# Kernel optimization log

Measured on AMD Instinct MI355X. Metric: run time of the kernel, lower is better.

## Reference

```python
import jax, jax.numpy as jnp
import numpy as np

B, LK, D, H = 16, 4096, 1024, 16
DK = D // H
EPS = 1e-5
NEG = -1.0e9


def _layernorm(x, g, b):
    m = jnp.mean(x, axis=-1, keepdims=True)
    v = jnp.mean((x - m) ** 2, axis=-1, keepdims=True)
    return (x - m) * jax.lax.rsqrt(v + EPS) * g + b


def setup_inputs() -> dict:
    key0 = jax.random.key(0)
    ks = jax.random.split(key0, 12)

    def lin(k, fan_in, fan_out):
        # torch nn.Linear default-ish scale; stored as [in, out] so y = x @ W + b
        return jax.random.normal(k, (fan_in, fan_out), jnp.float32) / np.float32(np.sqrt(fan_in))

    return {
        "query": jax.random.normal(ks[0], (B, 1, D), jnp.float32),
        "key": jax.random.normal(ks[1], (B, LK, D), jnp.float32),
        "mask": jax.random.randint(ks[2], (B, 1, LK), 0, 2, jnp.int32),
        "Wq": lin(ks[3], D, D), "bq": jnp.zeros((D,), jnp.float32),
        "Wk": lin(ks[4], D, D), "bk": jnp.zeros((D,), jnp.float32),
        "Wv": lin(ks[5], D, D), "bv": jnp.zeros((D,), jnp.float32),
        "Wo": lin(ks[6], D, D), "bo": jnp.zeros((D,), jnp.float32),
        "raw_thr": jnp.full((H, 1, 1), 0.1, jnp.float32),
        "Wvp": lin(ks[7], 2 * D, D),  # v_proj, no bias
        "W1": lin(ks[8], D, 2 * D), "b1": jnp.zeros((2 * D,), jnp.float32),
        "W2": lin(ks[9], 2 * D, D), "b2": jnp.zeros((D,), jnp.float32),
        "g1": jnp.ones((D,), jnp.float32), "be1": jnp.zeros((D,), jnp.float32),
        "g2": jnp.ones((D,), jnp.float32), "be2": jnp.zeros((D,), jnp.float32),
    }


def reference(query, key, mask, Wq, bq, Wk, bk, Wv, bv, Wo, bo, raw_thr,
              Wvp, W1, b1, W2, b2, g1, be1, g2, be2):
    b = query.shape[0]
    lk = key.shape[1]
    # v = cat(key, query.repeat(1, Lk, 1)) @ Wvp   (query has seq_len 1)
    v_in = jnp.concatenate([key, jnp.broadcast_to(query, (b, lk, D))], axis=2)
    v = v_in @ Wvp  # [B, Lk, D]

    Q = (query @ Wq + bq).reshape(b, 1, H, DK).transpose(0, 2, 1, 3)   # [B,H,1,DK]
    K = (key @ Wk + bk).reshape(b, lk, H, DK).transpose(0, 2, 1, 3)    # [B,H,Lk,DK]
    V = (v @ Wv + bv).reshape(b, lk, H, DK).transpose(0, 2, 1, 3)      # [B,H,Lk,DK]

    scores = jnp.einsum("bhqd,bhkd->bhqk", Q, K) / jnp.sqrt(jnp.float32(DK))
    # padding mask: [B,1,Lk] -> [B,1,1,Lk]
    scores = jnp.where(mask[:, None] == 0, NEG, scores)
    # learned per-head threshold: softplus(raw_thr) -> [1,H,1,1]
    thr = jax.nn.softplus(raw_thr)[None]
    scores = jnp.where(scores <= thr, NEG, scores)
    attn = jax.nn.softmax(scores, axis=-1)

    x = jnp.einsum("bhqk,bhkd->bhqd", attn, V)            # [B,H,1,DK]
    x = x.transpose(0, 2, 1, 3).reshape(b, 1, H * DK)      # [B,1,D]
    attn_out = x @ Wo + bo

    x = _layernorm(query + attn_out, g1, be1)
    ff = jax.nn.relu(x @ W1 + b1) @ W2 + b2
    x = _layernorm(x + ff, g2, be2)
    return x
```

## Files before the change

kernel.cpp:

```cpp
#include <hip/hip_runtime.h>
#include <hip/hip_bf16.h>

#define NB 16
#define NHD 16
#define ND 1024
#define NLK 4096
#define NFF 2048

typedef float f32x4 __attribute__((ext_vector_type(4)));
typedef __bf16 bf16x4v __attribute__((ext_vector_type(4)));
typedef __bf16 bf16x8 __attribute__((ext_vector_type(8)));

__global__ void k_fill(float* out, int n, float v) {
  int i = blockIdx.x * 256 + threadIdx.x;
  if (i < n) out[i] = v;
}

__global__ __launch_bounds__(256) void k0t(const float* __restrict__ Wvp,
                                           __hip_bfloat16* __restrict__ wvpt) {
  int n0 = blockIdx.x * 64, k0 = blockIdx.y * 64;
  int t = threadIdx.x;
  __shared__ float ts[64][68];
#pragma unroll
  for (int i = 0; i < 4; ++i) {
    int idx = t * 4 + i * 1024;
    int kk = idx >> 6, nn = idx & 63;
    float4 v = *(const float4*)(Wvp + (size_t)(k0 + kk) * ND + n0 + nn);
    ts[kk][nn] = v.x; ts[kk][nn + 1] = v.y; ts[kk][nn + 2] = v.z; ts[kk][nn + 3] = v.w;
  }
  __syncthreads();
#pragma unroll
  for (int i = 0; i < 4; ++i) {
    int idx = t * 4 + i * 1024;
    int nn = idx >> 6, kk = idx & 63;
    bf16x4v o;
#pragma unroll
    for (int j = 0; j < 4; ++j) o[j] = (__bf16)ts[kk + j][nn];
    *(bf16x4v*)((__bf16*)wvpt + (size_t)(n0 + nn) * ND + k0 + kk) = o;
  }
}

__global__ __launch_bounds__(256) void k0a(const float* __restrict__ Wq,
                                           const float* __restrict__ bq,
                                           const float* __restrict__ Wvp,
                                           const float* __restrict__ query,
                                           float* __restrict__ Qrow,
                                           float* __restrict__ cvec) {
  int which = blockIdx.z;
  int j = blockIdx.x * 256 + threadIdx.x;
  int i0 = blockIdx.y * 64;
  int t = threadIdx.x;
  __shared__ float qs[64][20];
  {
    int e = t * 4;
    int b = e >> 6, ii = e & 63;
    float4 v = *(const float4*)(query + (size_t)b * ND + i0 + ii);
    qs[ii][b] = v.x; qs[ii + 1][b] = v.y; qs[ii + 2][b] = v.z; qs[ii + 3][b] = v.w;
  }
  __syncthreads();
  float acc[16];
#pragma unroll
  for (int q = 0; q < 16; ++q) acc[q] = 0.f;
  for (int ii = 0; ii < 64; ++ii) {
    int i = i0 + ii;
    float wv = which ? Wvp[(size_t)(ND + i) * ND + j] : Wq[(size_t)i * ND + j];
    float qv[16];
    const float4* qp = (const float4*)&qs[ii][0];
    *(float4*)&qv[0] = qp[0];
    *(float4*)&qv[4] = qp[1];
    *(float4*)&qv[8] = qp[2];
    *(float4*)&qv[12] = qp[3];
#pragma unroll
    for (int q = 0; q < 16; ++q) acc[q] += wv * qv[q];
  }
  float* out = which ? cvec : Qrow;
  float bias = (!which && blockIdx.y == 0) ? bq[j] : 0.f;
#pragma unroll
  for (int q = 0; q < 16; ++q) atomicAdd(&out[q * ND + j], acc[q] + bias);
}

__global__ __launch_bounds__(256) void k0b(const float* __restrict__ Wk,
                                           const float* __restrict__ bk,
                                           const float* __restrict__ Qrow,
                                           __hip_bfloat16* __restrict__ t_bf,
                                           float* __restrict__ s0) {
  int h = blockIdx.x;
  int d0 = blockIdx.y * 128;
  int t = threadIdx.x;
  __shared__ float qs[16 * 64];
  __shared__ float wks[128 * 66];
  {
    int lin = t * 4;
    int b = lin >> 6, dk = lin & 63;
    *(float4*)&qs[b * 64 + dk] = *(const float4*)(Qrow + b * ND + h * 64 + dk);
  }
#pragma unroll
  for (int e = 0; e < 8; ++e) {
    int lin = e * 1024 + t * 4;
    int d = lin >> 6, dk = lin & 63;
    *(float4*)&wks[d * 66 + dk] = *(const float4*)(Wk + (size_t)(d0 + d) * ND + h * 64 + dk);
  }
  __syncthreads();
  if (blockIdx.y == 0 && t < 16) {
    float a = 0.f;
    const float* bkh = bk + h * 64;
    for (int jj = 0; jj < 64; ++jj) a += bkh[jj] * qs[t * 64 + jj];
    s0[t * 16 + h] = a;
  }
  int d = t >> 1, bh = (t & 1) * 8;
  float acc[8];
#pragma unroll
  for (int q = 0; q < 8; ++q) acc[q] = 0.f;
  for (int dk = 0; dk < 64; ++dk) {
    float wv = wks[d * 66 + dk];
#pragma unroll
    for (int q = 0; q < 8; ++q) acc[q] += wv * qs[(bh + q) * 64 + dk];
  }
#pragma unroll
  for (int q = 0; q < 8; ++q)
    t_bf[(size_t)((bh + q) * 16 + h) * ND + d0 + d] = (__hip_bfloat16)acc[q];
}

__global__ __launch_bounds__(256) void k_flash(const float* __restrict__ key,
                                               const __hip_bfloat16* __restrict__ t_bf,
                                               const float* __restrict__ s0,
                                               const float* __restrict__ raw_thr,
                                               const int* __restrict__ mask,
                                               float* __restrict__ pu,
                                               float* __restrict__ mloc,
                                               float* __restrict__ lloc) {
  int ch = blockIdx.x, b = blockIdx.y;
  int t = threadIdx.x;
  int wv = t >> 6, lane = t & 63, l15 = lane & 15, g4 = lane >> 4;
  __shared__ float ps[4][32][17];
  __shared__ float wls[32][16];
  __shared__ float red[16][16];
  __shared__ float mrun[16], lrun[16], fact[16], mnew_s[16], thv_s[16], s0_s[16];
  f32x4 pu_r[16];
#pragma unroll
  for (int h = 0; h < 16; ++h) pu_r[h] = (f32x4){0.f, 0.f, 0.f, 0.f};
  if (t < 16) {
    mrun[t] = -1.0e9f;
    lrun[t] = 0.f;
    thv_s[t] = log1pf(expf(raw_thr[t]));
    s0_s[t] = s0[b * 16 + t];
  }
  __syncthreads();
  const float* keyb = key + (size_t)b * NLK * ND;
  const __hip_bfloat16* tb = t_bf + (size_t)(b * 16 + l15) * ND;
  int dsl = wv * 256;
  int dlane = dsl + lane * 4;
  int k0c = ch * 128;
  for (int sp = 0; sp < 4; ++sp) {
    int ks0 = k0c + sp * 32;
    f32x4 acc0 = {0.f, 0.f, 0.f, 0.f}, acc1 = {0.f, 0.f, 0.f, 0.f};
    for (int st = 0; st < 8; ++st) {
      int d = dsl + st * 32 + g4 * 8;
      bf16x8 bfr = *(const bf16x8*)(tb + d);
      const float* a0p = keyb + (size_t)(ks0 + l15) * ND + d;
      const float* a1p = a0p + (size_t)16 * ND;
      float a0[8], a1[8];
      *(float4*)&a0[0] = *(const float4*)a0p;
      *(float4*)&a0[4] = *(const float4*)(a0p + 4);
      *(float4*)&a1[0] = *(const float4*)a1p;
      *(float4*)&a1[4] = *(const float4*)(a1p + 4);
      bf16x8 af0, af1;
#pragma unroll
      for (int j = 0; j < 8; ++j) {
        af0[j] = (__bf16)a0[j];
        af1[j] = (__bf16)a1[j];
      }
      acc0 = __builtin_amdgcn_mfma_f32_16x16x32_bf16(af0, bfr, acc0, 0, 0, 0);
      acc1 = __builtin_amdgcn_mfma_f32_16x16x32_bf16(af1, bfr, acc1, 0, 0, 0);
    }
#pragma unroll
    for (int r = 0; r < 4; ++r) {
      ps[wv][g4 * 4 + r][l15] = acc0[r];
      ps[wv][16 + g4 * 4 + r][l15] = acc1[r];
    }
    __syncthreads();
    int kk0 = t >> 4, hh = t & 15;
    float sv0, sv1;
    {
      float s = (ps[0][kk0][hh] + ps[1][kk0][hh] + ps[2][kk0][hh] + ps[3][kk0][hh] +
                 s0_s[hh]) * 0.125f;
      int mv = mask[b * NLK + ks0 + kk0];
      sv0 = (mv != 0 && s > thv_s[hh]) ? s : -1.0e9f;
    }
    {
      int k2 = kk0 + 16;
      float s = (ps[0][k2][hh] + ps[1][k2][hh] + ps[2][k2][hh] + ps[3][k2][hh] +
                 s0_s[hh]) * 0.125f;
      int mv = mask[b * NLK + ks0 + k2];
      sv1 = (mv != 0 && s > thv_s[hh]) ? s : -1.0e9f;
    }
    red[kk0][hh] = fmaxf(sv0, sv1);
    __syncthreads();
    for (int s2 = 8; s2 > 0; s2 >>= 1) {
      if (kk0 < s2) red[kk0][hh] = fmaxf(red[kk0][hh], red[kk0 + s2][hh]);
      __syncthreads();
    }
    if (t < 16) {
      float mn = fmaxf(mrun[t], red[0][t]);
      mnew_s[t] = mn;
      fact[t] = expf(mrun[t] - mn);
      mrun[t] = mn;
    }
    __syncthreads();
    float w0 = expf(sv0 - mnew_s[hh]);
    float w1 = expf(sv1 - mnew_s[hh]);
    wls[kk0][hh] = w0;
    wls[kk0 + 16][hh] = w1;
    red[kk0][hh] = w0 + w1;
    __syncthreads();
    for (int s2 = 8; s2 > 0; s2 >>= 1) {
      if (kk0 < s2) red[kk0][hh] += red[kk0 + s2][hh];
      __syncthreads();
    }
    if (t < 16) lrun[t] = lrun[t] * fact[t] + red[0][t];
#pragma unroll
    for (int h = 0; h < 16; ++h) pu_r[h] *= fact[h];
    const float* kb2 = keyb + (size_t)ks0 * ND + dlane;
    for (int k = 0; k < 32; ++k) {
      f32x4 kv = *(const f32x4*)(kb2 + (size_t)k * ND);
#pragma unroll
      for (int h = 0; h < 16; ++h) pu_r[h] += wls[k][h] * kv;
    }
    __syncthreads();
  }
  size_t pubase = (size_t)((b * 32 + ch) * 16) * ND + dlane;
#pragma unroll
  for (int h = 0; h < 16; ++h) *(f32x4*)(pu + pubase + (size_t)h * ND) = pu_r[h];
  if (t < 16) {
    mloc[(b * 32 + ch) * 16 + t] = mrun[t];
    lloc[(b * 32 + ch) * 16 + t] = lrun[t];
  }
}

__global__ __launch_bounds__(256) void k_ured(const float* __restrict__ pu,
                                              const float* __restrict__ mloc,
                                              const float* __restrict__ lloc,
                                              __hip_bfloat16* __restrict__ u_bf) {
  int h = blockIdx.x, b = blockIdx.y;
  int t = threadIdx.x;
  __shared__ float sc_s[32];
  if (t < 32) {
    float m = mloc[(b * 32 + t) * 16 + h];
    float l = lloc[(b * 32 + t) * 16 + h];
    float mg = m;
    for (int o = 16; o > 0; o >>= 1) mg = fmaxf(mg, __shfl_xor(mg, o, 32));
    float term = l * expf(m - mg);
    float ls = term;
    for (int o = 16; o > 0; o >>= 1) ls += __shfl_xor(ls, o, 32);
    sc_s[t] = expf(m - mg) / ls;
  }
  __syncthreads();
  int d = t * 4;
  f32x4 acc = {0.f, 0.f, 0.f, 0.f};
  for (int c = 0; c < 32; ++c) {
    f32x4 v = *(const f32x4*)(pu + (size_t)((b * 32 + c) * 16 + h) * ND + d);
    acc += sc_s[c] * v;
  }
  bf16x4v o;
#pragma unroll
  for (int j = 0; j < 4; ++j) o[j] = (__bf16)acc[j];
  *(bf16x4v*)((__bf16*)u_bf + (size_t)(b * 16 + h) * ND + d) = o;
}

__global__ __launch_bounds__(256) void k_zm(const __hip_bfloat16* __restrict__ u_bf,
                                            const __hip_bfloat16* __restrict__ wvpt,
                                            float* __restrict__ z) {
  int ntg = blockIdx.x, mt = blockIdx.y;
  int t = threadIdx.x, wv = t >> 6, lane = t & 63, l15 = lane & 15, g4 = lane >> 4;
  int nt = ntg * 4 + wv;
  const __hip_bfloat16* ub = u_bf + (size_t)(mt * 16 + l15) * ND;
  const __hip_bfloat16* wb = wvpt + (size_t)(nt * 16 + l15) * ND;
  f32x4 acc = {0.f, 0.f, 0.f, 0.f};
  for (int ks = 0; ks < 32; ++ks) {
    int d = ks * 32 + g4 * 8;
    bf16x8 a = *(const bf16x8*)(ub + d);
    bf16x8 bb = *(const bf16x8*)(wb + d);
    acc = __builtin_amdgcn_mfma_f32_16x16x32_bf16(a, bb, acc, 0, 0, 0);
  }
#pragma unroll
  for (int r = 0; r < 4; ++r)
    z[(size_t)(mt * 16 + g4 * 4 + r) * ND + nt * 16 + l15] = acc[r];
}

__global__ __launch_bounds__(256) void k_attnx(const float* __restrict__ z,
                                               const float* __restrict__ cvec,
                                               const float* __restrict__ Wv,
                                               const float* __restrict__ bv,
                                               float* __restrict__ attn_x) {
  __shared__ float vb[16 * 132];
  int h = blockIdx.x;
  int d0 = blockIdx.y * 128;
  int t = threadIdx.x;
#pragma unroll
  for (int e = 0; e < 8; ++e) {
    int lin = e * 256 + t;
    int bb = lin >> 7, dd = lin & 127;
    vb[bb * 132 + dd] =
        z[(size_t)(bb * 16 + h) * ND + d0 + dd] + cvec[(size_t)bb * ND + d0 + dd];
  }
  __syncthreads();
  int joff = t & 63, bg = t >> 6;
  int j = h * 64 + joff;
  float acc[4] = {0.f, 0.f, 0.f, 0.f};
  for (int dd = 0; dd < 128; ++dd) {
    float wv = Wv[(size_t)(d0 + dd) * ND + j];
#pragma unroll
    for (int q = 0; q < 4; ++q) acc[q] += wv * vb[(bg * 4 + q) * 132 + dd];
  }
#pragma unroll
  for (int q = 0; q < 4; ++q) {
    float val = acc[q];
    if (blockIdx.y == 0) val += bv[j];
    atomicAdd(&attn_x[(size_t)(bg * 4 + q) * ND + j], val);
  }
}

__global__ __launch_bounds__(256) void k_r1(const float* __restrict__ attn_x,
                                            const float* __restrict__ Wo,
                                            const float* __restrict__ bo,
                                            const float* __restrict__ query,
                                            float* __restrict__ r1) {
  __shared__ float ax[16 * 68];
  int j0 = blockIdx.x * 128;
  int d0 = blockIdx.y * 64;
  int t = threadIdx.x;
  {
    int lin = t * 4;
    int bb = lin >> 6, dd = lin & 63;
    *(float4*)&ax[bb * 68 + dd] = *(const float4*)(attn_x + (size_t)bb * ND + d0 + dd);
  }
  __syncthreads();
  int joff = t & 127, bg = t >> 7;
  int j = j0 + joff;
  float acc[8];
#pragma unroll
  for (int q = 0; q < 8; ++q) acc[q] = 0.f;
  for (int dd = 0; dd < 64; ++dd) {
    float wv = Wo[(size_t)(d0 + dd) * ND + j];
#pragma unroll
    for (int q = 0; q < 8; ++q) acc[q] += wv * ax[(bg * 8 + q) * 68 + dd];
  }
#pragma unroll
  for (int q = 0; q < 8; ++q) {
    int bb = bg * 8 + q;
    float val = acc[q];
    if (blockIdx.y == 0) val += bo[j] + query[(size_t)bb * ND + j];
    atomicAdd(&r1[(size_t)bb * ND + j], val);
  }
}

__global__ __launch_bounds__(256) void k_ff1(const float* __restrict__ r1,
                                             const float* __restrict__ g1,
                                             const float* __restrict__ be1,
                                             const float* __restrict__ W1,
                                             float* __restrict__ h1) {
  int n = blockIdx.x * 256 + threadIdx.x;
  int d0 = blockIdx.y * 64;
  int t = threadIdx.x;
  __shared__ float mv_s[16], iv_s[16];
  __shared__ float xs[16 * 68];
  {
    int row = t >> 4, seg = t & 15;
    float s = 0.f, s2 = 0.f;
    const float* rp = r1 + (size_t)row * ND + seg * 64;
    for (int q = 0; q < 16; ++q) {
      float4 v = *(const float4*)(rp + q * 4);
      s += v.x + v.y + v.z + v.w;
      s2 += v.x * v.x + v.y * v.y + v.z * v.z + v.w * v.w;
    }
    for (int o = 1; o < 16; o <<= 1) {
      s += __shfl_xor(s, o, 16);
      s2 += __shfl_xor(s2, o, 16);
    }
    if (seg == 0) {
      float mean = s * (1.f / ND);
      float var = s2 * (1.f / ND) - mean * mean;
      mv_s[row] = mean;
      iv_s[row] = rsqrtf(var + 1e-5f);
    }
  }
  __syncthreads();
  {
    int e = t * 4;
    int bb = e >> 6, dd = e & 63;
    float4 v = *(const float4*)(r1 + (size_t)bb * ND + d0 + dd);
    float4 g = *(const float4*)(g1 + d0 + dd);
    float4 be = *(const float4*)(be1 + d0 + dd);
    float m = mv_s[bb], iv = iv_s[bb];
    xs[bb * 68 + dd] = (v.x - m) * iv * g.x + be.x;
    xs[bb * 68 + dd + 1] = (v.y - m) * iv * g.y + be.y;
    xs[bb * 68 + dd + 2] = (v.z - m) * iv * g.z + be.z;
    xs[bb * 68 + dd + 3] = (v.w - m) * iv * g.w + be.w;
  }
  __syncthreads();
  float acc[16];
#pragma unroll
  for (int q = 0; q < 16; ++q) acc[q] = 0.f;
  for (int dd = 0; dd < 64; ++dd) {
    float wv = W1[(size_t)(d0 + dd) * NFF + n];
#pragma unroll
    for (int q = 0; q < 16; ++q) acc[q] += wv * xs[q * 68 + dd];
  }
#pragma unroll
  for (int q = 0; q < 16; ++q) atomicAdd(&h1[(size_t)q * NFF + n], acc[q]);
}

__global__ __launch_bounds__(256) void k_ff2(const float* __restrict__ h1,
                                             const float* __restrict__ b1,
                                             const float* __restrict__ W2,
                                             float* __restrict__ out2) {
  __shared__ float hs[16 * 132];
  int j0 = blockIdx.x * 128;
  int n0 = blockIdx.y * 128;
  int t = threadIdx.x;
#pragma unroll
  for (int e = 0; e < 8; ++e) {
    int lin = e * 256 + t;
    int bb = lin >> 7, nn = lin & 127;
    float hv = h1[(size_t)bb * NFF + n0 + nn] + b1[n0 + nn];
    hs[bb * 132 + nn] = fmaxf(hv, 0.f);
  }
  __syncthreads();
  int joff = t & 127, bg = t >> 7;
  int j = j0 + joff;
  float acc[8];
#pragma unroll
  for (int q = 0; q < 8; ++q) acc[q] = 0.f;
  for (int nn = 0; nn < 128; ++nn) {
    float wv = W2[(size_t)(n0 + nn) * ND + j];
#pragma unroll
    for (int q = 0; q < 8; ++q) acc[q] += wv * hs[(bg * 8 + q) * 132 + nn];
  }
#pragma unroll
  for (int q = 0; q < 8; ++q) atomicAdd(&out2[(size_t)(bg * 8 + q) * ND + j], acc[q]);
}

__global__ __launch_bounds__(256) void k_ln2(const float* __restrict__ r1,
                                             const float* __restrict__ g1,
                                             const float* __restrict__ be1,
                                             const float* __restrict__ out2,
                                             const float* __restrict__ b2,
                                             const float* __restrict__ g2,
                                             const float* __restrict__ be2,
                                             float* __restrict__ outp) {
  int b = blockIdx.x, t = threadIdx.x;
  __shared__ float rs[256], rs2[256];
  float4 v = *(const float4*)(r1 + (size_t)b * ND + t * 4);
  float s = v.x + v.y + v.z + v.w;
  float s2 = v.x * v.x + v.y * v.y + v.z * v.z + v.w * v.w;
  rs[t] = s;
  rs2[t] = s2;
  __syncthreads();
  for (int st = 128; st > 0; st >>= 1) {
    if (t < st) {
      rs[t] += rs[t + st];
      rs2[t] += rs2[t + st];
    }
    __syncthreads();
  }
  float mean = rs[0] * (1.f / ND);
  float var = rs2[0] * (1.f / ND) - mean * mean;
  float inv = rsqrtf(var + 1e-5f);
  float4 g = *(const float4*)(g1 + t * 4);
  float4 be = *(const float4*)(be1 + t * 4);
  float4 o2 = *(const float4*)(out2 + (size_t)b * ND + t * 4);
  float4 bb2 = *(const float4*)(b2 + t * 4);
  float4 v2;
  v2.x = (v.x - mean) * inv * g.x + be.x + o2.x + bb2.x;
  v2.y = (v.y - mean) * inv * g.y + be.y + o2.y + bb2.y;
  v2.z = (v.z - mean) * inv * g.z + be.z + o2.z + bb2.z;
  v2.w = (v.w - mean) * inv * g.w + be.w + o2.w + bb2.w;
  __syncthreads();
  s = v2.x + v2.y + v2.z + v2.w;
  s2 = v2.x * v2.x + v2.y * v2.y + v2.z * v2.z + v2.w * v2.w;
  rs[t] = s;
  rs2[t] = s2;
  __syncthreads();
  for (int st = 128; st > 0; st >>= 1) {
    if (t < st) {
      rs[t] += rs[t + st];
      rs2[t] += rs2[t + st];
    }
    __syncthreads();
  }
  float mean2 = rs[0] * (1.f / ND);
  float var2 = rs2[0] * (1.f / ND) - mean2 * mean2;
  float inv2 = rsqrtf(var2 + 1e-5f);
  float4 gg = *(const float4*)(g2 + t * 4);
  float4 bbe = *(const float4*)(be2 + t * 4);
  float4 o;
  o.x = (v2.x - mean2) * inv2 * gg.x + bbe.x;
  o.y = (v2.y - mean2) * inv2 * gg.y + bbe.y;
  o.z = (v2.z - mean2) * inv2 * gg.z + bbe.z;
  o.w = (v2.w - mean2) * inv2 * gg.w + bbe.w;
  *(float4*)(outp + (size_t)b * ND + t * 4) = o;
}

extern "C" void kernel_launch(void* const* d_in, const int* in_sizes, int n_in,
                              void* d_out, int out_size, void* d_ws, size_t ws_size,
                              hipStream_t stream) {
  const float* query = (const float*)d_in[0];
  const float* key = (const float*)d_in[1];
  const int* mask = (const int*)d_in[2];
  const float* Wq = (const float*)d_in[3];
  const float* bq = (const float*)d_in[4];
  const float* Wk = (const float*)d_in[5];
  const float* bk = (const float*)d_in[6];
  const float* Wv = (const float*)d_in[7];
  const float* bv = (const float*)d_in[8];
  const float* Wo = (const float*)d_in[9];
  const float* bo = (const float*)d_in[10];
  const float* raw_thr = (const float*)d_in[11];
  const float* Wvp = (const float*)d_in[12];
  const float* W1 = (const float*)d_in[13];
  const float* b1 = (const float*)d_in[14];
  const float* W2 = (const float*)d_in[15];
  const float* b2 = (const float*)d_in[16];
  const float* g1 = (const float*)d_in[17];
  const float* be1 = (const float*)d_in[18];
  const float* g2 = (const float*)d_in[19];
  const float* be2 = (const float*)d_in[20];

  const size_t OFF_QROW = 0;
  const size_t OFF_C = 65536;
  const size_t OFF_ATTNX = 131072;
  const size_t OFF_R1 = 196608;
  const size_t OFF_H1 = 262144;
  const size_t OFF_OUT2 = 393216;
  const size_t ZERO_BYTES = 458752;
  const size_t OFF_S0 = 458752;
  const size_t OFF_MLOC = 459776;
  const size_t OFF_LLOC = 492544;
  const size_t OFF_TBF = 525312;
  const size_t OFF_UBF = 1049600;
  const size_t OFF_WVPT = 1573888;
  const size_t OFF_Z = 3671040;
  const size_t OFF_PU = 4719616;
  const size_t TOTAL = 38274048;

  if (ws_size < TOTAL) {
    k_fill<<<dim3((out_size + 255) / 256), dim3(256), 0, stream>>>((float*)d_out, out_size,
                                                                   12345.0f);
    return;
  }

  char* wsb = (char*)d_ws;
  float* Qrow = (float*)(wsb + OFF_QROW);
  float* cvec = (float*)(wsb + OFF_C);
  float* attn_x = (float*)(wsb + OFF_ATTNX);
  float* r1 = (float*)(wsb + OFF_R1);
  float* h1 = (float*)(wsb + OFF_H1);
  float* out2 = (float*)(wsb + OFF_OUT2);
  float* s0 = (float*)(wsb + OFF_S0);
  float* mloc = (float*)(wsb + OFF_MLOC);
  float* lloc = (float*)(wsb + OFF_LLOC);
  __hip_bfloat16* t_bf = (__hip_bfloat16*)(wsb + OFF_TBF);
  __hip_bfloat16* u_bf = (__hip_bfloat16*)(wsb + OFF_UBF);
  __hip_bfloat16* wvpt = (__hip_bfloat16*)(wsb + OFF_WVPT);
  float* z = (float*)(wsb + OFF_Z);
  float* pu = (float*)(wsb + OFF_PU);

  hipMemsetAsync(d_ws, 0, ZERO_BYTES, stream);

  k0t<<<dim3(16, 16), dim3(256), 0, stream>>>(Wvp, wvpt);
  k0a<<<dim3(4, 16, 2), dim3(256), 0, stream>>>(Wq, bq, Wvp, query, Qrow, cvec);
  k0b<<<dim3(16, 8), dim3(256), 0, stream>>>(Wk, bk, Qrow, t_bf, s0);
  k_flash<<<dim3(32, 16), dim3(256), 0, stream>>>(key, t_bf, s0, raw_thr, mask, pu, mloc, lloc);
  k_ured<<<dim3(16, 16), dim3(256), 0, stream>>>(pu, mloc, lloc, u_bf);
  k_zm<<<dim3(16, 16), dim3(256), 0, stream>>>(u_bf, wvpt, z);
  k_attnx<<<dim3(16, 8), dim3(256), 0, stream>>>(z, cvec, Wv, bv, attn_x);
  k_r1<<<dim3(8, 16), dim3(256), 0, stream>>>(attn_x, Wo, bo, query, r1);
  k_ff1<<<dim3(8, 16), dim3(256), 0, stream>>>(r1, g1, be1, W1, h1);
  k_ff2<<<dim3(8, 16), dim3(256), 0, stream>>>(h1, b1, W2, out2);
  k_ln2<<<dim3(16), dim3(256), 0, stream>>>(r1, g1, be1, out2, b2, g2, be2, (float*)d_out);
}
```

Before: 205.2 us.

## Fuse tail stages into persistent kernel with grid barriers; widen flash blocks

Merges the Wvp transpose and the query projections into one prep kernel. Seven tail kernels (u reduction, z GEMM, attn_x, r1, ff1, ff2, ln2) become a single 256-block kernel that uses atomic-counter grid barriers in place of kernel launches. k_flash now uses 512 threads with 8 waves, each covering half the d-slice, and its per-step max/sum reductions use wave shuffles instead of log-step shared-memory loops. This removes launch gaps and trims register pressure in flash. The grid barriers can deadlock if the 256 blocks are not all resident at once, and the flash block now has a larger cross-wave partial-sum reduction.

```diff
diff --git a/kernel.cpp b/kernel.cpp
--- a/kernel.cpp
+++ b/kernel.cpp
@@ -8,6 +8,7 @@
 #define NFF 2048
 
 typedef float f32x4 __attribute__((ext_vector_type(4)));
+typedef float f32x2 __attribute__((ext_vector_type(2)));
 typedef __bf16 bf16x4v __attribute__((ext_vector_type(4)));
 typedef __bf16 bf16x8 __attribute__((ext_vector_type(8)));
 
@@ -16,67 +17,91 @@
   if (i < n) out[i] = v;
 }
 
-__global__ __launch_bounds__(256) void k0t(const float* __restrict__ Wvp,
-                                           __hip_bfloat16* __restrict__ wvpt) {
-  int n0 = blockIdx.x * 64, k0 = blockIdx.y * 64;
+__device__ __forceinline__ void gbar(unsigned* ctr, unsigned nblk) {
+  __syncthreads();
+  if (threadIdx.x == 0) {
+    __threadfence();
+    __hip_atomic_fetch_add(ctr, 1u, __ATOMIC_ACQ_REL, __HIP_MEMORY_SCOPE_AGENT);
+    while (__hip_atomic_load(ctr, __ATOMIC_ACQUIRE, __HIP_MEMORY_SCOPE_AGENT) < nblk) {
+    }
+    __threadfence();
+  }
+  __syncthreads();
+}
+
+__global__ __launch_bounds__(256) void k_prep(const float* __restrict__ Wq,
+                                              const float* __restrict__ bq,
+                                              const float* __restrict__ Wvp,
+                                              const float* __restrict__ query,
+                                              float* __restrict__ Qrow,
+                                              float* __restrict__ cvec,
+                                              __hip_bfloat16* __restrict__ wvpt) {
+  __shared__ float pmem[64 * 68];
+  int blk = blockIdx.x;
   int t = threadIdx.x;
-  __shared__ float ts[64][68];
-#pragma unroll
-  for (int i = 0; i < 4; ++i) {
-    int idx = t * 4 + i * 1024;
-    int kk = idx >> 6, nn = idx & 63;
-    float4 v = *(const float4*)(Wvp + (size_t)(k0 + kk) * ND + n0 + nn);
-    ts[kk][nn] = v.x; ts[kk][nn + 1] = v.y; ts[kk][nn + 2] = v.z; ts[kk][nn + 3] = v.w;
-  }
-  __syncthreads();
-#pragma unroll
-  for (int i = 0; i < 4; ++i) {
-    int idx = t * 4 + i * 1024;
-    int nn = idx >> 6, kk = idx & 63;
-    bf16x4v o;
-#pragma unroll
-    for (int j = 0; j < 4; ++j) o[j] = (__bf16)ts[kk + j][nn];
-    *(bf16x4v*)((__bf16*)wvpt + (size_t)(n0 + nn) * ND + k0 + kk) = o;
-  }
-}
-
-__global__ __launch_bounds__(256) void k0a(const float* __restrict__ Wq,
-                                           const float* __restrict__ bq,
-                                           const float* __restrict__ Wvp,
-                                           const float* __restrict__ query,
-                                           float* __restrict__ Qrow,
-                                           float* __restrict__ cvec) {
-  int which = blockIdx.z;
-  int j = blockIdx.x * 256 + threadIdx.x;
-  int i0 = blockIdx.y * 64;
-  int t = threadIdx.x;
-  __shared__ float qs[64][20];
-  {
-    int e = t * 4;
-    int b = e >> 6, ii = e & 63;
-    float4 v = *(const float4*)(query + (size_t)b * ND + i0 + ii);
-    qs[ii][b] = v.x; qs[ii + 1][b] = v.y; qs[ii + 2][b] = v.z; qs[ii + 3][b] = v.w;
-  }
-  __syncthreads();
-  float acc[16];
-#pragma unroll
-  for (int q = 0; q < 16; ++q) acc[q] = 0.f;
-  for (int ii = 0; ii < 64; ++ii) {
-    int i = i0 + ii;
-    float wv = which ? Wvp[(size_t)(ND + i) * ND + j] : Wq[(size_t)i * ND + j];
-    float qv[16];
-    const float4* qp = (const float4*)&qs[ii][0];
-    *(float4*)&qv[0] = qp[0];
-    *(float4*)&qv[4] = qp[1];
-    *(float4*)&qv[8] = qp[2];
-    *(float4*)&qv[12] = qp[3];
-#pragma unroll
-    for (int q = 0; q < 16; ++q) acc[q] += wv * qv[q];
-  }
-  float* out = which ? cvec : Qrow;
-  float bias = (!which && blockIdx.y == 0) ? bq[j] : 0.f;
-#pragma unroll
-  for (int q = 0; q < 16; ++q) atomicAdd(&out[q * ND + j], acc[q] + bias);
+  if (blk < 128) {
+    int which = blk >> 6;
+    int jb = blk & 3;
+    int i0 = ((blk >> 2) & 15) * 64;
+    int j = jb * 256 + t;
+    {
+      int e = t * 4;
+      int b = e >> 6, ii = e & 63;
+      float4 v = *(const float4*)(query + (size_t)b * ND + i0 + ii);
+      pmem[ii * 20 + b] = v.x;
+      pmem[(ii + 1) * 20 + b] = v.y;
+      pmem[(ii + 2) * 20 + b] = v.z;
+      pmem[(ii + 3) * 20 + b] = v.w;
+    }
+    __syncthreads();
+    float acc[16];
+#pragma unroll
+    for (int q = 0; q < 16; ++q) acc[q] = 0.f;
+    for (int ii = 0; ii < 64; ++ii) {
+      int i = i0 + ii;
+      float wv = which ? Wvp[(size_t)(ND + i) * ND + j] : Wq[(size_t)i * ND + j];
+      float qv[16];
+      const float4* qp = (const float4*)&pmem[ii * 20];
+      *(float4*)&qv[0] = qp[0];
+      *(float4*)&qv[4] = qp[1];
+      *(float4*)&qv[8] = qp[2];
+      *(float4*)&qv[12] = qp[3];
+#pragma unroll
+      for (int q = 0; q < 16; ++q) acc[q] += wv * qv[q];
+    }
+    float* out = which ? cvec : Qrow;
+    float bias = (!which && i0 == 0) ? bq[j] : 0.f;
+#pragma unroll
+    for (int q = 0; q < 16; ++q) atomicAdd(&out[q * ND + j], acc[q] + bias);
+  } else {
+    int tb = blk - 128;
+    int n0 = (tb & 15) * 64;
+    int k0base = (tb >> 4) * 256;
+    for (int it = 0; it < 4; ++it) {
+      int k0 = k0base + it * 64;
+#pragma unroll
+      for (int i = 0; i < 4; ++i) {
+        int idx = t * 4 + i * 1024;
+        int kk = idx >> 6, nn = idx & 63;
+        float4 v = *(const float4*)(Wvp + (size_t)(k0 + kk) * ND + n0 + nn);
+        pmem[kk * 68 + nn] = v.x;
+        pmem[kk * 68 + nn + 1] = v.y;
+        pmem[kk * 68 + nn + 2] = v.z;
+        pmem[kk * 68 + nn + 3] = v.w;
+      }
+      __syncthreads();
+#pragma unroll
+      for (int i = 0; i < 4; ++i) {
+        int idx = t * 4 + i * 1024;
+        int nn = idx >> 6, kk = idx & 63;
+        bf16x4v o;
+#pragma unroll
+        for (int j = 0; j < 4; ++j) o[j] = (__bf16)pmem[(kk + j) * 68 + nn];
+        *(bf16x4v*)((__bf16*)wvpt + (size_t)(n0 + nn) * ND + k0 + kk) = o;
+      }
+      __syncthreads();
+    }
+  }
 }
 
 __global__ __launch_bounds__(256) void k0b(const float* __restrict__ Wk,
@@ -121,24 +146,24 @@
     t_bf[(size_t)((bh + q) * 16 + h) * ND + d0 + d] = (__hip_bfloat16)acc[q];
 }
 
-__global__ __launch_bounds__(256) void k_flash(const float* __restrict__ key,
-                                               const __hip_bfloat16* __restrict__ t_bf,
-                                               const float* __restrict__ s0,
-                                               const float* __restrict__ raw_thr,
-                                               const int* __restrict__ mask,
-                                               float* __restrict__ pu,
-                                               float* __restrict__ mloc,
-                                               float* __restrict__ lloc) {
+__global__ __launch_bounds__(512, 4) void k_flash(const float* __restrict__ key,
+                                                  const __hip_bfloat16* __restrict__ t_bf,
+                                                  const float* __restrict__ s0,
+                                                  const float* __restrict__ raw_thr,
+                                                  const int* __restrict__ mask,
+                                                  float* __restrict__ pu,
+                                                  float* __restrict__ mloc,
+                                                  float* __restrict__ lloc) {
   int ch = blockIdx.x, b = blockIdx.y;
   int t = threadIdx.x;
   int wv = t >> 6, lane = t & 63, l15 = lane & 15, g4 = lane >> 4;
-  __shared__ float ps[4][32][17];
+  __shared__ float ps[8][32][17];
+  __shared__ float scr[32][17];
   __shared__ float wls[32][16];
-  __shared__ float red[16][16];
   __shared__ float mrun[16], lrun[16], fact[16], mnew_s[16], thv_s[16], s0_s[16];
-  f32x4 pu_r[16];
-#pragma unroll
-  for (int h = 0; h < 16; ++h) pu_r[h] = (f32x4){0.f, 0.f, 0.f, 0.f};
+  f32x2 pu_r[16];
+#pragma unroll
+  for (int h = 0; h < 16; ++h) pu_r[h] = (f32x2){0.f, 0.f};
   if (t < 16) {
     mrun[t] = -1.0e9f;
     lrun[t] = 0.f;
@@ -148,13 +173,14 @@
   __syncthreads();
   const float* keyb = key + (size_t)b * NLK * ND;
   const __hip_bfloat16* tb = t_bf + (size_t)(b * 16 + l15) * ND;
-  int dsl = wv * 256;
-  int dlane = dsl + lane * 4;
-  int k0c = ch * 128;
+  int dsl = wv * 128;
+  int dlane = dsl + lane * 2;
+  int kk = t >> 4, hh = t & 15;
   for (int sp = 0; sp < 4; ++sp) {
-    int ks0 = k0c + sp * 32;
+    int ks0 = ch * 128 + sp * 32;
     f32x4 acc0 = {0.f, 0.f, 0.f, 0.f}, acc1 = {0.f, 0.f, 0.f, 0.f};
-    for (int st = 0; st < 8; ++st) {
+#pragma unroll
+    for (int st = 0; st < 4; ++st) {
       int d = dsl + st * 32 + g4 * 8;
       bf16x8 bfr = *(const bf16x8*)(tb + d);
       const float* a0p = keyb + (size_t)(ks0 + l15) * ND + d;
@@ -179,326 +205,329 @@
       ps[wv][16 + g4 * 4 + r][l15] = acc1[r];
     }
     __syncthreads();
-    int kk0 = t >> 4, hh = t & 15;
-    float sv0, sv1;
+    float sv;
     {
-      float s = (ps[0][kk0][hh] + ps[1][kk0][hh] + ps[2][kk0][hh] + ps[3][kk0][hh] +
-                 s0_s[hh]) * 0.125f;
-      int mv = mask[b * NLK + ks0 + kk0];
-      sv0 = (mv != 0 && s > thv_s[hh]) ? s : -1.0e9f;
-    }
-    {
-      int k2 = kk0 + 16;
-      float s = (ps[0][k2][hh] + ps[1][k2][hh] + ps[2][k2][hh] + ps[3][k2][hh] +
-                 s0_s[hh]) * 0.125f;
-      int mv = mask[b * NLK + ks0 + k2];
-      sv1 = (mv != 0 && s > thv_s[hh]) ? s : -1.0e9f;
-    }
-    red[kk0][hh] = fmaxf(sv0, sv1);
-    __syncthreads();
-    for (int s2 = 8; s2 > 0; s2 >>= 1) {
-      if (kk0 < s2) red[kk0][hh] = fmaxf(red[kk0][hh], red[kk0 + s2][hh]);
-      __syncthreads();
-    }
-    if (t < 16) {
-      float mn = fmaxf(mrun[t], red[0][t]);
-      mnew_s[t] = mn;
-      fact[t] = expf(mrun[t] - mn);
-      mrun[t] = mn;
-    }
-    __syncthreads();
-    float w0 = expf(sv0 - mnew_s[hh]);
-    float w1 = expf(sv1 - mnew_s[hh]);
-    wls[kk0][hh] = w0;
-    wls[kk0 + 16][hh] = w1;
-    red[kk0][hh] = w0 + w1;
-    __syncthreads();
-    for (int s2 = 8; s2 > 0; s2 >>= 1) {
-      if (kk0 < s2) red[kk0][hh] += red[kk0 + s2][hh];
-      __syncthreads();
-    }
-    if (t < 16) lrun[t] = lrun[t] * fact[t] + red[0][t];
+      float sum = 0.f;
+#pragma unroll
+      for (int w = 0; w < 8; ++w) sum += ps[w][kk][hh];
+      float sc_ = (sum + s0_s[hh]) * 0.125f;
+      int mv = mask[b * NLK + ks0 + kk];
+      sv = (mv != 0 && sc_ > thv_s[hh]) ? sc_ : -1.0e9f;
+      scr[kk][hh] = sv;
+    }
+    __syncthreads();
+    if (wv == 0) {
+      float m = -3.4e38f;
+#pragma unroll
+      for (int j = 0; j < 8; ++j) m = fmaxf(m, scr[g4 * 8 + j][l15]);
+      m = fmaxf(m, __shfl_xor(m, 16, 64));
+      m = fmaxf(m, __shfl_xor(m, 32, 64));
+      if (lane < 16) {
+        float mn = fmaxf(mrun[lane], m);
+        mnew_s[lane] = mn;
+        fact[lane] = expf(mrun[lane] - mn);
+        mrun[lane] = mn;
+      }
+    }
+    __syncthreads();
+    float w = expf(sv - mnew_s[hh]);
+    wls[kk][hh] = w;
+    scr[kk][hh] = w;
+    __syncthreads();
+    if (wv == 0) {
+      float s = 0.f;
+#pragma unroll
+      for (int j = 0; j < 8; ++j) s += scr[g4 * 8 + j][l15];
+      s += __shfl_xor(s, 16, 64);
+      s += __shfl_xor(s, 32, 64);
+      if (lane < 16) lrun[lane] = lrun[lane] * fact[lane] + s;
+    }
 #pragma unroll
     for (int h = 0; h < 16; ++h) pu_r[h] *= fact[h];
     const float* kb2 = keyb + (size_t)ks0 * ND + dlane;
     for (int k = 0; k < 32; ++k) {
-      f32x4 kv = *(const f32x4*)(kb2 + (size_t)k * ND);
-#pragma unroll
-      for (int h = 0; h < 16; ++h) pu_r[h] += wls[k][h] * kv;
-    }
-    __syncthreads();
+      f32x2 kv = *(const f32x2*)(kb2 + (size_t)k * ND);
+      const f32x4* wr = (const f32x4*)&wls[k][0];
+      f32x4 w0 = wr[0], w1 = wr[1], w2 = wr[2], w3 = wr[3];
+#pragma unroll
+      for (int q = 0; q < 4; ++q) {
+        pu_r[q] += w0[q] * kv;
+        pu_r[4 + q] += w1[q] * kv;
+        pu_r[8 + q] += w2[q] * kv;
+        pu_r[12 + q] += w3[q] * kv;
+      }
+    }
   }
   size_t pubase = (size_t)((b * 32 + ch) * 16) * ND + dlane;
 #pragma unroll
-  for (int h = 0; h < 16; ++h) *(f32x4*)(pu + pubase + (size_t)h * ND) = pu_r[h];
+  for (int h = 0; h < 16; ++h) *(f32x2*)(pu + pubase + (size_t)h * ND) = pu_r[h];
   if (t < 16) {
     mloc[(b * 32 + ch) * 16 + t] = mrun[t];
     lloc[(b * 32 + ch) * 16 + t] = lrun[t];
   }
 }
 
-__global__ __launch_bounds__(256) void k_ured(const float* __restrict__ pu,
-                                              const float* __restrict__ mloc,
-                                              const float* __restrict__ lloc,
-                                              __hip_bfloat16* __restrict__ u_bf) {
-  int h = blockIdx.x, b = blockIdx.y;
-  int t = threadIdx.x;
-  __shared__ float sc_s[32];
-  if (t < 32) {
-    float m = mloc[(b * 32 + t) * 16 + h];
-    float l = lloc[(b * 32 + t) * 16 + h];
-    float mg = m;
-    for (int o = 16; o > 0; o >>= 1) mg = fmaxf(mg, __shfl_xor(mg, o, 32));
-    float term = l * expf(m - mg);
-    float ls = term;
-    for (int o = 16; o > 0; o >>= 1) ls += __shfl_xor(ls, o, 32);
-    sc_s[t] = expf(m - mg) / ls;
-  }
-  __syncthreads();
-  int d = t * 4;
-  f32x4 acc = {0.f, 0.f, 0.f, 0.f};
-  for (int c = 0; c < 32; ++c) {
-    f32x4 v = *(const f32x4*)(pu + (size_t)((b * 32 + c) * 16 + h) * ND + d);
-    acc += sc_s[c] * v;
-  }
-  bf16x4v o;
-#pragma unroll
-  for (int j = 0; j < 4; ++j) o[j] = (__bf16)acc[j];
-  *(bf16x4v*)((__bf16*)u_bf + (size_t)(b * 16 + h) * ND + d) = o;
-}
-
-__global__ __launch_bounds__(256) void k_zm(const __hip_bfloat16* __restrict__ u_bf,
-                                            const __hip_bfloat16* __restrict__ wvpt,
-                                            float* __restrict__ z) {
-  int ntg = blockIdx.x, mt = blockIdx.y;
-  int t = threadIdx.x, wv = t >> 6, lane = t & 63, l15 = lane & 15, g4 = lane >> 4;
-  int nt = ntg * 4 + wv;
-  const __hip_bfloat16* ub = u_bf + (size_t)(mt * 16 + l15) * ND;
-  const __hip_bfloat16* wb = wvpt + (size_t)(nt * 16 + l15) * ND;
-  f32x4 acc = {0.f, 0.f, 0.f, 0.f};
-  for (int ks = 0; ks < 32; ++ks) {
-    int d = ks * 32 + g4 * 8;
-    bf16x8 a = *(const bf16x8*)(ub + d);
-    bf16x8 bb = *(const bf16x8*)(wb + d);
-    acc = __builtin_amdgcn_mfma_f32_16x16x32_bf16(a, bb, acc, 0, 0, 0);
-  }
-#pragma unroll
-  for (int r = 0; r < 4; ++r)
-    z[(size_t)(mt * 16 + g4 * 4 + r) * ND + nt * 16 + l15] = acc[r];
-}
-
-__global__ __launch_bounds__(256) void k_attnx(const float* __restrict__ z,
-                                               const float* __restrict__ cvec,
-                                               const float* __restrict__ Wv,
-                                               const float* __restrict__ bv,
-                                               float* __restrict__ attn_x) {
-  __shared__ float vb[16 * 132];
-  int h = blockIdx.x;
-  int d0 = blockIdx.y * 128;
-  int t = threadIdx.x;
-#pragma unroll
-  for (int e = 0; e < 8; ++e) {
-    int lin = e * 256 + t;
-    int bb = lin >> 7, dd = lin & 127;
-    vb[bb * 132 + dd] =
-        z[(size_t)(bb * 16 + h) * ND + d0 + dd] + cvec[(size_t)bb * ND + d0 + dd];
-  }
-  __syncthreads();
-  int joff = t & 63, bg = t >> 6;
-  int j = h * 64 + joff;
-  float acc[4] = {0.f, 0.f, 0.f, 0.f};
-  for (int dd = 0; dd < 128; ++dd) {
-    float wv = Wv[(size_t)(d0 + dd) * ND + j];
-#pragma unroll
-    for (int q = 0; q < 4; ++q) acc[q] += wv * vb[(bg * 4 + q) * 132 + dd];
-  }
-#pragma unroll
-  for (int q = 0; q < 4; ++q) {
-    float val = acc[q];
-    if (blockIdx.y == 0) val += bv[j];
-    atomicAdd(&attn_x[(size_t)(bg * 4 + q) * ND + j], val);
-  }
-}
-
-__global__ __launch_bounds__(256) void k_r1(const float* __restrict__ attn_x,
-                                            const float* __restrict__ Wo,
-                                            const float* __restrict__ bo,
-                                            const float* __restrict__ query,
-                                            float* __restrict__ r1) {
-  __shared__ float ax[16 * 68];
-  int j0 = blockIdx.x * 128;
-  int d0 = blockIdx.y * 64;
-  int t = threadIdx.x;
+__global__ __launch_bounds__(256) void k_tail(
+    const float* __restrict__ pu, const float* __restrict__ mloc,
+    const float* __restrict__ lloc, __hip_bfloat16* __restrict__ u_bf,
+    const __hip_bfloat16* __restrict__ wvpt, float* __restrict__ z,
+    const float* __restrict__ cvec, const float* __restrict__ Wv,
+    const float* __restrict__ bv, float* __restrict__ attn_x,
+    const float* __restrict__ Wo, const float* __restrict__ bo,
+    const float* __restrict__ query, float* __restrict__ r1,
+    const float* __restrict__ g1, const float* __restrict__ be1,
+    const float* __restrict__ W1, float* __restrict__ h1,
+    const float* __restrict__ b1, const float* __restrict__ W2,
+    float* __restrict__ out2, const float* __restrict__ b2,
+    const float* __restrict__ g2, const float* __restrict__ be2,
+    float* __restrict__ outp, unsigned* __restrict__ ctr) {
+  __shared__ float smf[2176];
+  int blk = blockIdx.x, t = threadIdx.x;
+  int wv = t >> 6, lane = t & 63, l15 = lane & 15, g4 = lane >> 4;
+
   {
-    int lin = t * 4;
-    int bb = lin >> 6, dd = lin & 63;
-    *(float4*)&ax[bb * 68 + dd] = *(const float4*)(attn_x + (size_t)bb * ND + d0 + dd);
-  }
-  __syncthreads();
-  int joff = t & 127, bg = t >> 7;
-  int j = j0 + joff;
-  float acc[8];
-#pragma unroll
-  for (int q = 0; q < 8; ++q) acc[q] = 0.f;
-  for (int dd = 0; dd < 64; ++dd) {
-    float wv = Wo[(size_t)(d0 + dd) * ND + j];
-#pragma unroll
-    for (int q = 0; q < 8; ++q) acc[q] += wv * ax[(bg * 8 + q) * 68 + dd];
-  }
-#pragma unroll
-  for (int q = 0; q < 8; ++q) {
-    int bb = bg * 8 + q;
-    float val = acc[q];
-    if (blockIdx.y == 0) val += bo[j] + query[(size_t)bb * ND + j];
-    atomicAdd(&r1[(size_t)bb * ND + j], val);
-  }
-}
-
-__global__ __launch_bounds__(256) void k_ff1(const float* __restrict__ r1,
-                                             const float* __restrict__ g1,
-                                             const float* __restrict__ be1,
-                                             const float* __restrict__ W1,
-                                             float* __restrict__ h1) {
-  int n = blockIdx.x * 256 + threadIdx.x;
-  int d0 = blockIdx.y * 64;
-  int t = threadIdx.x;
-  __shared__ float mv_s[16], iv_s[16];
-  __shared__ float xs[16 * 68];
+    int g = blk * 256 + t;
+    if (g < 16384) {
+      attn_x[g] = 0.f;
+      r1[g] = 0.f;
+      out2[g] = 0.f;
+    }
+    if (g < 32768) h1[g] = 0.f;
+    int b = blk >> 4, h = blk & 15;
+    if (t < 32) {
+      float m = mloc[(b * 32 + t) * 16 + h];
+      float l = lloc[(b * 32 + t) * 16 + h];
+      float mg = m;
+      for (int o = 16; o > 0; o >>= 1) mg = fmaxf(mg, __shfl_xor(mg, o, 32));
+      float term = l * expf(m - mg);
+      float ls = term;
+      for (int o = 16; o > 0; o >>= 1) ls += __shfl_xor(ls, o, 32);
+      smf[t] = expf(m - mg) / ls;
+    }
+    __syncthreads();
+    int d = t * 4;
+    f32x4 acc = {0.f, 0.f, 0.f, 0.f};
+    for (int c = 0; c < 32; ++c) {
+      f32x4 v = *(const f32x4*)(pu + (size_t)((b * 32 + c) * 16 + h) * ND + d);
+      acc += smf[c] * v;
+    }
+    bf16x4v o;
+#pragma unroll
+    for (int j = 0; j < 4; ++j) o[j] = (__bf16)acc[j];
+    *(bf16x4v*)((__bf16*)u_bf + (size_t)(b * 16 + h) * ND + d) = o;
+  }
+  gbar(&ctr[0], 256);
+
   {
-    int row = t >> 4, seg = t & 15;
-    float s = 0.f, s2 = 0.f;
-    const float* rp = r1 + (size_t)row * ND + seg * 64;
-    for (int q = 0; q < 16; ++q) {
-      float4 v = *(const float4*)(rp + q * 4);
-      s += v.x + v.y + v.z + v.w;
-      s2 += v.x * v.x + v.y * v.y + v.z * v.z + v.w * v.w;
-    }
-    for (int o = 1; o < 16; o <<= 1) {
-      s += __shfl_xor(s, o, 16);
-      s2 += __shfl_xor(s2, o, 16);
-    }
-    if (seg == 0) {
-      float mean = s * (1.f / ND);
-      float var = s2 * (1.f / ND) - mean * mean;
-      mv_s[row] = mean;
-      iv_s[row] = rsqrtf(var + 1e-5f);
-    }
-  }
-  __syncthreads();
+    int ntg = blk & 15, mt = blk >> 4;
+    int nt = ntg * 4 + wv;
+    const __hip_bfloat16* ub = u_bf + (size_t)(mt * 16 + l15) * ND;
+    const __hip_bfloat16* wb = wvpt + (size_t)(nt * 16 + l15) * ND;
+    f32x4 acc = {0.f, 0.f, 0.f, 0.f};
+    for (int ks = 0; ks < 32; ++ks) {
+      int d = ks * 32 + g4 * 8;
+      bf16x8 a = *(const bf16x8*)(ub + d);
+      bf16x8 bb = *(const bf16x8*)(wb + d);
+      acc = __builtin_amdgcn_mfma_f32_16x16x32_bf16(a, bb, acc, 0, 0, 0);
+    }
+#pragma unroll
+    for (int r = 0; r < 4; ++r)
+      z[(size_t)(mt * 16 + g4 * 4 + r) * ND + nt * 16 + l15] = acc[r];
+  }
+  gbar(&ctr[1], 256);
+
   {
-    int e = t * 4;
-    int bb = e >> 6, dd = e & 63;
-    float4 v = *(const float4*)(r1 + (size_t)bb * ND + d0 + dd);
-    float4 g = *(const float4*)(g1 + d0 + dd);
-    float4 be = *(const float4*)(be1 + d0 + dd);
-    float m = mv_s[bb], iv = iv_s[bb];
-    xs[bb * 68 + dd] = (v.x - m) * iv * g.x + be.x;
-    xs[bb * 68 + dd + 1] = (v.y - m) * iv * g.y + be.y;
-    xs[bb * 68 + dd + 2] = (v.z - m) * iv * g.z + be.z;
-    xs[bb * 68 + dd + 3] = (v.w - m) * iv * g.w + be.w;
-  }
-  __syncthreads();
-  float acc[16];
-#pragma unroll
-  for (int q = 0; q < 16; ++q) acc[q] = 0.f;
-  for (int dd = 0; dd < 64; ++dd) {
-    float wv = W1[(size_t)(d0 + dd) * NFF + n];
-#pragma unroll
-    for (int q = 0; q < 16; ++q) acc[q] += wv * xs[q * 68 + dd];
-  }
-#pragma unroll
-  for (int q = 0; q < 16; ++q) atomicAdd(&h1[(size_t)q * NFF + n], acc[q]);
-}
-
-__global__ __launch_bounds__(256) void k_ff2(const float* __restrict__ h1,
-                                             const float* __restrict__ b1,
-                                             const float* __restrict__ W2,
-                                             float* __restrict__ out2) {
-  __shared__ float hs[16 * 132];
-  int j0 = blockIdx.x * 128;
-  int n0 = blockIdx.y * 128;
-  int t = threadIdx.x;
-#pragma unroll
-  for (int e = 0; e < 8; ++e) {
-    int lin = e * 256 + t;
-    int bb = lin >> 7, nn = lin & 127;
-    float hv = h1[(size_t)bb * NFF + n0 + nn] + b1[n0 + nn];
-    hs[bb * 132 + nn] = fmaxf(hv, 0.f);
-  }
-  __syncthreads();
-  int joff = t & 127, bg = t >> 7;
-  int j = j0 + joff;
-  float acc[8];
-#pragma unroll
-  for (int q = 0; q < 8; ++q) acc[q] = 0.f;
-  for (int nn = 0; nn < 128; ++nn) {
-    float wv = W2[(size_t)(n0 + nn) * ND + j];
-#pragma unroll
-    for (int q = 0; q < 8; ++q) acc[q] += wv * hs[(bg * 8 + q) * 132 + nn];
-  }
-#pragma unroll
-  for (int q = 0; q < 8; ++q) atomicAdd(&out2[(size_t)(bg * 8 + q) * ND + j], acc[q]);
-}
-
-__global__ __launch_bounds__(256) void k_ln2(const float* __restrict__ r1,
-                                             const float* __restrict__ g1,
-                                             const float* __restrict__ be1,
-                                             const float* __restrict__ out2,
-                                             const float* __restrict__ b2,
-                                             const float* __restrict__ g2,
-                                             const float* __restrict__ be2,
-                                             float* __restrict__ outp) {
-  int b = blockIdx.x, t = threadIdx.x;
-  __shared__ float rs[256], rs2[256];
-  float4 v = *(const float4*)(r1 + (size_t)b * ND + t * 4);
-  float s = v.x + v.y + v.z + v.w;
-  float s2 = v.x * v.x + v.y * v.y + v.z * v.z + v.w * v.w;
-  rs[t] = s;
-  rs2[t] = s2;
-  __syncthreads();
-  for (int st = 128; st > 0; st >>= 1) {
-    if (t < st) {
-      rs[t] += rs[t + st];
-      rs2[t] += rs2[t + st];
-    }
-    __syncthreads();
-  }
-  float mean = rs[0] * (1.f / ND);
-  float var = rs2[0] * (1.f / ND) - mean * mean;
-  float inv = rsqrtf(var + 1e-5f);
-  float4 g = *(const float4*)(g1 + t * 4);
-  float4 be = *(const float4*)(be1 + t * 4);
-  float4 o2 = *(const float4*)(out2 + (size_t)b * ND + t * 4);
-  float4 bb2 = *(const float4*)(b2 + t * 4);
-  float4 v2;
-  v2.x = (v.x - mean) * inv * g.x + be.x + o2.x + bb2.x;
-  v2.y = (v.y - mean) * inv * g.y + be.y + o2.y + bb2.y;
-  v2.z = (v.z - mean) * inv * g.z + be.z + o2.z + bb2.z;
-  v2.w = (v.w - mean) * inv * g.w + be.w + o2.w + bb2.w;
-  __syncthreads();
-  s = v2.x + v2.y + v2.z + v2.w;
-  s2 = v2.x * v2.x + v2.y * v2.y + v2.z * v2.z + v2.w * v2.w;
-  rs[t] = s;
-  rs2[t] = s2;
-  __syncthreads();
-  for (int st = 128; st > 0; st >>= 1) {
-    if (t < st) {
-      rs[t] += rs[t + st];
-      rs2[t] += rs2[t + st];
-    }
-    __syncthreads();
-  }
-  float mean2 = rs[0] * (1.f / ND);
-  float var2 = rs2[0] * (1.f / ND) - mean2 * mean2;
-  float inv2 = rsqrtf(var2 + 1e-5f);
-  float4 gg = *(const float4*)(g2 + t * 4);
-  float4 bbe = *(const float4*)(be2 + t * 4);
-  float4 o;
-  o.x = (v2.x - mean2) * inv2 * gg.x + bbe.x;
-  o.y = (v2.y - mean2) * inv2 * gg.y + bbe.y;
-  o.z = (v2.z - mean2) * inv2 * gg.z + bbe.z;
-  o.w = (v2.w - mean2) * inv2 * gg.w + bbe.w;
-  *(float4*)(outp + (size_t)b * ND + t * 4) = o;
+    int h = blk >> 4, d0 = (blk & 15) * 64;
+    float* vb = smf;
+#pragma unroll
+    for (int e = 0; e < 4; ++e) {
+      int lin = e * 256 + t;
+      int bb = lin >> 6, dd = lin & 63;
+      vb[bb * 68 + dd] =
+          z[(size_t)(bb * 16 + h) * ND + d0 + dd] + cvec[(size_t)bb * ND + d0 + dd];
+    }
+    __syncthreads();
+    int joff = t & 63, bg = t >> 6;
+    int j = h * 64 + joff;
+    float acc[4] = {0.f, 0.f, 0.f, 0.f};
+    for (int dd = 0; dd < 64; ++dd) {
+      float wv_ = Wv[(size_t)(d0 + dd) * ND + j];
+#pragma unroll
+      for (int q = 0; q < 4; ++q) acc[q] += wv_ * vb[(bg * 4 + q) * 68 + dd];
+    }
+#pragma unroll
+    for (int q = 0; q < 4; ++q) {
+      float val = acc[q];
+      if ((blk & 15) == 0) val += bv[j];
+      atomicAdd(&attn_x[(size_t)(bg * 4 + q) * ND + j], val);
+    }
+  }
+  gbar(&ctr[2], 256);
+
+  if (blk < 128) {
+    int j0 = (blk & 7) * 128;
+    int d0 = (blk >> 3) * 64;
+    float* ax = smf;
+    {
+      int lin = t * 4;
+      int bb = lin >> 6, dd = lin & 63;
+      *(float4*)&ax[bb * 68 + dd] = *(const float4*)(attn_x + (size_t)bb * ND + d0 + dd);
+    }
+    __syncthreads();
+    int joff = t & 127, bg = t >> 7;
+    int j = j0 + joff;
+    float acc[8];
+#pragma unroll
+    for (int q = 0; q < 8; ++q) acc[q] = 0.f;
+    for (int dd = 0; dd < 64; ++dd) {
+      float wv_ = Wo[(size_t)(d0 + dd) * ND + j];
+#pragma unroll
+      for (int q = 0; q < 8; ++q) acc[q] += wv_ * ax[(bg * 8 + q) * 68 + dd];
+    }
+#pragma unroll
+    for (int q = 0; q < 8; ++q) {
+      int bb = bg * 8 + q;
+      float val = acc[q];
+      if ((blk >> 3) == 0) val += bo[j] + query[(size_t)bb * ND + j];
+      atomicAdd(&r1[(size_t)bb * ND + j], val);
+    }
+  }
+  gbar(&ctr[3], 256);
+
+  if (blk < 128) {
+    int n = (blk & 7) * 256 + t;
+    int d0 = (blk >> 3) * 64;
+    float* xs = smf;
+    float* mv_s = smf + 1984;
+    float* iv_s = smf + 2000;
+    {
+      int row = t >> 4, seg = t & 15;
+      float s = 0.f, s2 = 0.f;
+      const float* rp = r1 + (size_t)row * ND + seg * 64;
+      for (int q = 0; q < 16; ++q) {
+        float4 v = *(const float4*)(rp + q * 4);
+        s += v.x + v.y + v.z + v.w;
+        s2 += v.x * v.x + v.y * v.y + v.z * v.z + v.w * v.w;
+      }
+      for (int o = 1; o < 16; o <<= 1) {
+        s += __shfl_xor(s, o, 16);
+        s2 += __shfl_xor(s2, o, 16);
+      }
+      if (seg == 0) {
+        float mean = s * (1.f / ND);
+        float var = s2 * (1.f / ND) - mean * mean;
+        mv_s[row] = mean;
+        iv_s[row] = rsqrtf(var + 1e-5f);
+      }
+    }
+    __syncthreads();
+    {
+      int e = t * 4;
+      int bb = e >> 6, dd = e & 63;
+      float4 v = *(const float4*)(r1 + (size_t)bb * ND + d0 + dd);
+      float4 g = *(const float4*)(g1 + d0 + dd);
+      float4 be = *(const float4*)(be1 + d0 + dd);
+      float m = mv_s[bb], iv = iv_s[bb];
+      xs[bb * 68 + dd] = (v.x - m) * iv * g.x + be.x;
+      xs[bb * 68 + dd + 1] = (v.y - m) * iv * g.y + be.y;
+      xs[bb * 68 + dd + 2] = (v.z - m) * iv * g.z + be.z;
+      xs[bb * 68 + dd + 3] = (v.w - m) * iv * g.w + be.w;
+    }
+    __syncthreads();
+    float acc[16];
+#pragma unroll
+    for (int q = 0; q < 16; ++q) acc[q] = 0.f;
+    for (int dd = 0; dd < 64; ++dd) {
+      float wv_ = W1[(size_t)(d0 + dd) * NFF + n];
+#pragma unroll
+      for (int q = 0; q < 16; ++q) acc[q] += wv_ * xs[q * 68 + dd];
+    }
+#pragma unroll
+    for (int q = 0; q < 16; ++q) atomicAdd(&h1[(size_t)q * NFF + n], acc[q]);
+  }
+  gbar(&ctr[4], 256);
+
+  if (blk < 128) {
+    int j0 = (blk & 7) * 128;
+    int n0 = (blk >> 3) * 128;
+    float* hs = smf;
+#pragma unroll
+    for (int e = 0; e < 8; ++e) {
+      int lin = e * 256 + t;
+      int bb = lin >> 7, nn = lin & 127;
+      float hv = h1[(size_t)bb * NFF + n0 + nn] + b1[n0 + nn];
+      hs[bb * 132 + nn] = fmaxf(hv, 0.f);
+    }
+    __syncthreads();
+    int joff = t & 127, bg = t >> 7;
+    int j = j0 + joff;
+    float acc[8];
+#pragma unroll
+    for (int q = 0; q < 8; ++q) acc[q] = 0.f;
+    for (int nn = 0; nn < 128; ++nn) {
+      float wv_ = W2[(size_t)(n0 + nn) * ND + j];
+#pragma unroll
+      for (int q = 0; q < 8; ++q) acc[q] += wv_ * hs[(bg * 8 + q) * 132 + nn];
+    }
+#pragma unroll
+    for (int q = 0; q < 8; ++q) atomicAdd(&out2[(size_t)(bg * 8 + q) * ND + j], acc[q]);
+  }
+  gbar(&ctr[5], 256);
+
+  if (blk < 16) {
+    int b = blk;
+    float* rs = smf;
+    float* rs2 = smf + 256;
+    float4 v = *(const float4*)(r1 + (size_t)b * ND + t * 4);
+    float s = v.x + v.y + v.z + v.w;
+    float s2 = v.x * v.x + v.y * v.y + v.z * v.z + v.w * v.w;
+    rs[t] = s;
+    rs2[t] = s2;
+    __syncthreads();
+    for (int st = 128; st > 0; st >>= 1) {
+      if (t < st) {
+        rs[t] += rs[t + st];
+        rs2[t] += rs2[t + st];
+      }
+      __syncthreads();
+    }
+    float mean = rs[0] * (1.f / ND);
+    float var = rs2[0] * (1.f / ND) - mean * mean;
+    float inv = rsqrtf(var + 1e-5f);
+    float4 g = *(const float4*)(g1 + t * 4);
+    float4 be = *(const float4*)(be1 + t * 4);
+    float4 o2 = *(const float4*)(out2 + (size_t)b * ND + t * 4);
+    float4 bb2 = *(const float4*)(b2 + t * 4);
+    float4 v2;
+    v2.x = (v.x - mean) * inv * g.x + be.x + o2.x + bb2.x;
+    v2.y = (v.y - mean) * inv * g.y + be.y + o2.y + bb2.y;
+    v2.z = (v.z - mean) * inv * g.z + be.z + o2.z + bb2.z;
+    v2.w = (v.w - mean) * inv * g.w + be.w + o2.w + bb2.w;
+    __syncthreads();
+    s = v2.x + v2.y + v2.z + v2.w;
+    s2 = v2.x * v2.x + v2.y * v2.y + v2.z * v2.z + v2.w * v2.w;
+    rs[t] = s;
+    rs2[t] = s2;
+    __syncthreads();
+    for (int st = 128; st > 0; st >>= 1) {
+      if (t < st) {
+        rs[t] += rs[t + st];
+        rs2[t] += rs2[t + st];
+      }
+      __syncthreads();
+    }
+    float mean2 = rs[0] * (1.f / ND);
+    float var2 = rs2[0] * (1.f / ND) - mean2 * mean2;
+    float inv2 = rsqrtf(var2 + 1e-5f);
+    float4 gg = *(const float4*)(g2 + t * 4);
+    float4 bbe = *(const float4*)(be2 + t * 4);
+    float4 o;
+    o.x = (v2.x - mean2) * inv2 * gg.x + bbe.x;
+    o.y = (v2.y - mean2) * inv2 * gg.y + bbe.y;
+    o.z = (v2.z - mean2) * inv2 * gg.z + bbe.z;
+    o.w = (v2.w - mean2) * inv2 * gg.w + bbe.w;
+    *(float4*)(outp + (size_t)b * ND + t * 4) = o;
+  }
 }
 
 extern "C" void kernel_launch(void* const* d_in, const int* in_sizes, int n_in,
@@ -528,20 +557,21 @@
 
   const size_t OFF_QROW = 0;
   const size_t OFF_C = 65536;
-  const size_t OFF_ATTNX = 131072;
-  const size_t OFF_R1 = 196608;
-  const size_t OFF_H1 = 262144;
-  const size_t OFF_OUT2 = 393216;
-  const size_t ZERO_BYTES = 458752;
-  const size_t OFF_S0 = 458752;
-  const size_t OFF_MLOC = 459776;
-  const size_t OFF_LLOC = 492544;
-  const size_t OFF_TBF = 525312;
-  const size_t OFF_UBF = 1049600;
-  const size_t OFF_WVPT = 1573888;
-  const size_t OFF_Z = 3671040;
-  const size_t OFF_PU = 4719616;
-  const size_t TOTAL = 38274048;
+  const size_t OFF_CTR = 131072;
+  const size_t ZERO_BYTES = 132096;
+  const size_t OFF_ATTNX = 132096;
+  const size_t OFF_R1 = 197632;
+  const size_t OFF_H1 = 263168;
+  const size_t OFF_OUT2 = 394240;
+  const size_t OFF_S0 = 459776;
+  const size_t OFF_MLOC = 460800;
+  const size_t OFF_LLOC = 493568;
+  const size_t OFF_TBF = 526336;
+  const size_t OFF_UBF = 1050624;
+  const size_t OFF_WVPT = 1574912;
+  const size_t OFF_Z = 3672064;
+  const size_t OFF_PU = 4720640;
+  const size_t TOTAL = 38275072;
 
   if (ws_size < TOTAL) {
     k_fill<<<dim3((out_size + 255) / 256), dim3(256), 0, stream>>>((float*)d_out, out_size,
@@ -552,6 +582,7 @@
   char* wsb = (char*)d_ws;
   float* Qrow = (float*)(wsb + OFF_QROW);
   float* cvec = (float*)(wsb + OFF_C);
+  unsigned* ctr = (unsigned*)(wsb + OFF_CTR);
   float* attn_x = (float*)(wsb + OFF_ATTNX);
   float* r1 = (float*)(wsb + OFF_R1);
   float* h1 = (float*)(wsb + OFF_H1);
@@ -567,15 +598,10 @@
 
   hipMemsetAsync(d_ws, 0, ZERO_BYTES, stream);
 
-  k0t<<<dim3(16, 16), dim3(256), 0, stream>>>(Wvp, wvpt);
-  k0a<<<dim3(4, 16, 2), dim3(256), 0, stream>>>(Wq, bq, Wvp, query, Qrow, cvec);
+  k_prep<<<dim3(192), dim3(256), 0, stream>>>(Wq, bq, Wvp, query, Qrow, cvec, wvpt);
   k0b<<<dim3(16, 8), dim3(256), 0, stream>>>(Wk, bk, Qrow, t_bf, s0);
-  k_flash<<<dim3(32, 16), dim3(256), 0, stream>>>(key, t_bf, s0, raw_thr, mask, pu, mloc, lloc);
-  k_ured<<<dim3(16, 16), dim3(256), 0, stream>>>(pu, mloc, lloc, u_bf);
-  k_zm<<<dim3(16, 16), dim3(256), 0, stream>>>(u_bf, wvpt, z);
-  k_attnx<<<dim3(16, 8), dim3(256), 0, stream>>>(z, cvec, Wv, bv, attn_x);
-  k_r1<<<dim3(8, 16), dim3(256), 0, stream>>>(attn_x, Wo, bo, query, r1);
-  k_ff1<<<dim3(8, 16), dim3(256), 0, stream>>>(r1, g1, be1, W1, h1);
-  k_ff2<<<dim3(8, 16), dim3(256), 0, stream>>>(h1, b1, W2, out2);
-  k_ln2<<<dim3(16), dim3(256), 0, stream>>>(r1, g1, be1, out2, b2, g2, be2, (float*)d_out);
+  k_flash<<<dim3(32, 16), dim3(512), 0, stream>>>(key, t_bf, s0, raw_thr, mask, pu, mloc, lloc);
+  k_tail<<<dim3(256), dim3(256), 0, stream>>>(pu, mloc, lloc, u_bf, wvpt, z, cvec, Wv, bv,
+                                              attn_x, Wo, bo, query, r1, g1, be1, W1, h1, b1,
+                                              W2, out2, b2, g2, be2, (float*)d_out, ctr);
 }
```

Result: slower. 375.3 us (+82.9%).
